# Optimization experiments

Hardware: AMD Instinct MI355X
Metric: run time of the kernel (lower is better)

The kernel has to match this reference:

```python
import jax, jax.numpy as jnp
import numpy as np

N_OUT, D_OUT, N_IN, D_IN, N_ROUTING = 32, 32, 2048, 16, 3
BATCH = 64


def squash(x, axis=-1):
    norm2 = jnp.sum(x * x, axis=axis, keepdims=True)
    scale = norm2 / (1.0 + norm2) / jnp.sqrt(norm2)
    return scale * x


def setup_inputs() -> dict:
    key = jax.random.key(0)
    k_u, k_w = jax.random.split(key)
    u = jax.random.normal(k_u, (BATCH, N_IN, D_IN), dtype=jnp.float32)
    stdv = 1.0 / np.sqrt(N_IN)
    W = jax.random.uniform(k_w, (N_IN, D_IN, N_OUT * D_OUT), dtype=jnp.float32,
                           minval=-stdv, maxval=stdv)
    return {"u": u, "W": W}


def reference(u, W):
    B = u.shape[0]
    # uhat[b,n,o,k] = sum_i u[b,n,i] * W[n,i,o*k]
    uhat = jnp.einsum('bni,nij->bnj', u, W).reshape(B, N_IN, N_OUT, D_OUT)
    b = jnp.zeros((B, N_IN, N_OUT), dtype=u.dtype)
    v = None
    for r in range(N_ROUTING):
        c = jax.nn.softmax(b, axis=-1)            # [B, nIn, nOut]
        s = jnp.einsum('bno,bnok->bok', c, uhat)  # [B, nOut, dOut]
        v = squash(s)
        if r != N_ROUTING - 1:
            a = jnp.einsum('bnok,bok->bno', uhat, v)  # agreement
            b = b + a
    return v
```

## Files before the change

kernel.cpp:

```cpp
#include <hip/hip_runtime.h>
#include <math.h>

#define N_OUT 32
#define D_OUT 32
#define N_IN 2048
#define D_IN 16
#define BATCH 64
#define J 1024

typedef __attribute__((ext_vector_type(8))) short short8;
typedef __attribute__((ext_vector_type(4))) float f32x4;
typedef __attribute__((ext_vector_type(16))) float f32x16;

__device__ __forceinline__ unsigned short f2bf(float f) {
  unsigned int x = __float_as_uint(f);
  return (unsigned short)((x + 0x7FFFu + ((x >> 16) & 1u)) >> 16);
}

__device__ __forceinline__ int wp(int u) { return u ^ ((u >> 3) & 1); }

__device__ __forceinline__ void pack_col(const float* wc, uint4& d0, uint4& d1) {
  d0.x = (unsigned)f2bf(wc[0])  | ((unsigned)f2bf(wc[1])  << 16);
  d0.y = (unsigned)f2bf(wc[2])  | ((unsigned)f2bf(wc[3])  << 16);
  d0.z = (unsigned)f2bf(wc[4])  | ((unsigned)f2bf(wc[5])  << 16);
  d0.w = (unsigned)f2bf(wc[6])  | ((unsigned)f2bf(wc[7])  << 16);
  d1.x = (unsigned)f2bf(wc[8])  | ((unsigned)f2bf(wc[9])  << 16);
  d1.y = (unsigned)f2bf(wc[10]) | ((unsigned)f2bf(wc[11]) << 16);
  d1.z = (unsigned)f2bf(wc[12]) | ((unsigned)f2bf(wc[13]) << 16);
  d1.w = (unsigned)f2bf(wc[14]) | ((unsigned)f2bf(wc[15]) << 16);
}

__device__ __forceinline__ short8 pack_u(const float4& a4, const float4& b4) {
  short8 B;
  B[0] = (short)f2bf(a4.x); B[1] = (short)f2bf(a4.y);
  B[2] = (short)f2bf(a4.z); B[3] = (short)f2bf(a4.w);
  B[4] = (short)f2bf(b4.x); B[5] = (short)f2bf(b4.y);
  B[6] = (short)f2bf(b4.z); B[7] = (short)f2bf(b4.w);
  return B;
}

__device__ __forceinline__ f32x16 zero16() {
  f32x16 z;
  #pragma unroll
  for (int i = 0; i < 16; ++i) z[i] = 0.f;
  return z;
}


template<int MODE>
__global__ __launch_bounds__(1024, 1)
void pass0w_kernel(const float* __restrict__ uf, const float* __restrict__ Wf,
                   short* __restrict__ Wbf, short* __restrict__ ubf,
                   float* __restrict__ part)
{
  __shared__ uint4 Wt[4][2048];

  const int t  = threadIdx.x;
  const int l  = t & 63;
  const int w  = t >> 6;
  const int bid = blockIdx.x;
  const int bh = (bid >> 3) & 1;
  const int cx = (bid & 7) | ((bid >> 4) << 3);
  const int n0 = cx * 16;

  const int bl = l & 31;
  const int b  = bh * 32 + bl;
  const int kh = l >> 5;
  const bool wq = (MODE == 0) && ((t >> 9) == bh);
  const bool uq = (MODE == 0) && (w == 0);

  int aoff[2];
  #pragma unroll
  for (int q = 0; q < 2; ++q) aoff[q] = wp(2 * (w * 64 + q * 32 + bl) + kh);

  f32x16 acc[2];
  acc[0] = zero16();
  acc[1] = zero16();

  short8 Ba, Bb;

  {
    float wa[16], wb[16];
    const float* sa = Wf + (size_t)n0 * (D_IN * J) + t;
    const float* sb = Wf + (size_t)(n0 + 1) * (D_IN * J) + t;
    #pragma unroll
    for (int i = 0; i < 16; ++i) wa[i] = sa[i * J];
    #pragma unroll
    for (int i = 0; i < 16; ++i) wb[i] = sb[i * J];
    const float* upa = uf + ((size_t)b * N_IN + n0) * D_IN + kh * 8;
    float4 ua0 = *reinterpret_cast<const float4*>(upa);
    float4 ua1 = *reinterpret_cast<const float4*>(upa + 4);
    const float* upb = uf + ((size_t)b * N_IN + n0 + 1) * D_IN + kh * 8;
    float4 ub0 = *reinterpret_cast<const float4*>(upb);
    float4 ub1 = *reinterpret_cast<const float4*>(upb + 4);
    __builtin_amdgcn_sched_barrier(0);
    uint4 d0, d1;
    pack_col(wa, d0, d1);
    Wt[0][wp(2 * t)] = d0;
    Wt[0][wp(2 * t + 1)] = d1;
    if (wq) {
      uint4* g = reinterpret_cast<uint4*>(Wbf + (size_t)n0 * (D_IN * J));
      g[wp(2 * t)] = d0;
      g[wp(2 * t + 1)] = d1;
    }
    pack_col(wb, d0, d1);
    Wt[1][wp(2 * t)] = d0;
    Wt[1][wp(2 * t + 1)] = d1;
    if (wq) {
      uint4* g = reinterpret_cast<uint4*>(Wbf + (size_t)(n0 + 1) * (D_IN * J));
      g[wp(2 * t)] = d0;
      g[wp(2 * t + 1)] = d1;
    }
    Ba = pack_u(ua0, ua1);
    Bb = pack_u(ub0, ub1);
    if (uq) {
      *reinterpret_cast<short8*>(ubf + ((size_t)b * N_IN + n0) * D_IN + kh * 8) = Ba;
      *reinterpret_cast<short8*>(ubf + ((size_t)b * N_IN + n0 + 1) * D_IN + kh * 8) = Bb;
    }
  }
  __syncthreads();

  for (int ss = 0; ss < 8; ++ss) {
    const int na = n0 + 2 * ss;
    const int p = ss & 1;
    const bool more = (ss + 1 < 8);

    float wa[16], wb[16];
    float4 ua0 = {0,0,0,0}, ua1 = {0,0,0,0}, ub0 = {0,0,0,0}, ub1 = {0,0,0,0};
    if (more) {
      const float* sa = Wf + (size_t)(na + 2) * (D_IN * J) + t;
      const float* sb = Wf + (size_t)(na + 3) * (D_IN * J) + t;
      #pragma unroll
      for (int i = 0; i < 16; ++i) wa[i] = sa[i * J];
      #pragma unroll
      for (int i = 0; i < 16; ++i) wb[i] = sb[i * J];
      const float* upa = uf + ((size_t)b * N_IN + na + 2) * D_IN + kh * 8;
      ua0 = *reinterpret_cast<const float4*>(upa);
      ua1 = *reinterpret_cast<const float4*>(upa + 4);
      const float* upb = uf + ((size_t)b * N_IN + na + 3) * D_IN + kh * 8;
      ub0 = *reinterpret_cast<const float4*>(upb);
      ub1 = *reinterpret_cast<const float4*>(upb + 4);
      __builtin_amdgcn_sched_barrier(0);
    }

    {
      const uint4* bufA = Wt[2 * p];
      const uint4* bufB = Wt[2 * p + 1];
      #pragma unroll
      for (int q = 0; q < 2; ++q) {
        short8 A = *reinterpret_cast<const short8*>(&bufA[aoff[q]]);
        acc[q] = __builtin_amdgcn_mfma_f32_32x32x16_bf16(A, Ba, acc[q], 0, 0, 0);
      }
      #pragma unroll
      for (int q = 0; q < 2; ++q) {
        short8 A = *reinterpret_cast<const short8*>(&bufB[aoff[q]]);
        acc[q] = __builtin_amdgcn_mfma_f32_32x32x16_bf16(A, Bb, acc[q], 0, 0, 0);
      }
    }

    short8 Bna, Bnb;
    if (more) {
      uint4 d0, d1;
      pack_col(wa, d0, d1);
      Wt[2 * (1 - p)][wp(2 * t)] = d0;
      Wt[2 * (1 - p)][wp(2 * t + 1)] = d1;
      if (wq) {
        uint4* g = reinterpret_cast<uint4*>(Wbf + (size_t)(na + 2) * (D_IN * J));
        g[wp(2 * t)] = d0;
        g[wp(2 * t + 1)] = d1;
      }
      pack_col(wb, d0, d1);
      Wt[2 * (1 - p) + 1][wp(2 * t)] = d0;
      Wt[2 * (1 - p) + 1][wp(2 * t + 1)] = d1;
      if (wq) {
        uint4* g = reinterpret_cast<uint4*>(Wbf + (size_t)(na + 3) * (D_IN * J));
        g[wp(2 * t)] = d0;
        g[wp(2 * t + 1)] = d1;
      }
      Bna = pack_u(ua0, ua1);
      Bnb = pack_u(ub0, ub1);
      if (uq) {
        *reinterpret_cast<short8*>(ubf + ((size_t)b * N_IN + na + 2) * D_IN + kh * 8) = Bna;
        *reinterpret_cast<short8*>(ubf + ((size_t)b * N_IN + na + 3) * D_IN + kh * 8) = Bnb;
      }
      Ba = Bna;
      Bb = Bnb;
    }
    __syncthreads();
  }

  #pragma unroll
  for (int q = 0; q < 2; ++q) {
    #pragma unroll
    for (int r = 0; r < 16; ++r) {
      int j = w * 64 + q * 32 + (r & 3) + 8 * (r >> 2) + 4 * kh;
      part[((size_t)cx * J + j) * 64 + b] = acc[q][r];
    }
  }
}

__global__ __launch_bounds__(1024, 1)
void pass1w_kernel(const short* __restrict__ Wbf, const short* __restrict__ ubf,
                   const float* __restrict__ vin, float* __restrict__ part)
{
  __shared__ uint4 Wt[2][2048];
  __shared__ float al[2][32][33];

  const int t  = threadIdx.x;
  const int l  = t & 63;
  const int w  = t >> 6;
  const int bid = blockIdx.x;
  const int bh = (bid >> 3) & 1;
  const int cx = (bid & 7) | ((bid >> 4) << 3);
  const int n0 = cx * 16;

  const int bl = l & 31;
  const int b  = bh * 32 + bl;
  const int kh = l >> 5;

  int aoff[2];
  #pragma unroll
  for (int q = 0; q < 2; ++q) aoff[q] = wp(2 * (w * 64 + q * 32 + bl) + kh);

  unsigned vb[16];
  #pragma unroll
  for (int q = 0; q < 2; ++q) {
    #pragma unroll
    for (int g = 0; g < 4; ++g) {
      int j = w * 64 + q * 32 + 8 * g + 4 * kh;
      f32x4 v4 = *reinterpret_cast<const f32x4*>(vin + (size_t)b * J + j);
      vb[q * 8 + 2 * g]     = (unsigned)f2bf(v4[0]) | ((unsigned)f2bf(v4[1]) << 16);
      vb[q * 8 + 2 * g + 1] = (unsigned)f2bf(v4[2]) | ((unsigned)f2bf(v4[3]) << 16);
    }
  }

  f32x16 acc[2];
  acc[0] = zero16();
  acc[1] = zero16();

  short8 B;
  {
    const uint4* src = reinterpret_cast<const uint4*>(Wbf + (size_t)n0 * (D_IN * J));
    Wt[0][t] = src[t];
    Wt[0][t + 1024] = src[t + 1024];
    B = *reinterpret_cast<const short8*>(ubf + ((size_t)b * N_IN + n0) * D_IN + kh * 8);
  }
  __syncthreads();

  for (int nn = 0; nn < 16; ++nn) {
    const int n = n0 + nn;
    const int cur = nn & 1, nxt = cur ^ 1, par = nn & 1;
    const bool more = (nn + 1 < 16);

    uint4 s0, s1;
    short8 Bn;
    if (more) {
      const uint4* src = reinterpret_cast<const uint4*>(Wbf + (size_t)(n + 1) * (D_IN * J));
      s0 = src[t];
      s1 = src[t + 1024];
      Bn = *reinterpret_cast<const short8*>(ubf + ((size_t)b * N_IN + n + 1) * D_IN + kh * 8);
      __builtin_amdgcn_sched_barrier(0);
    }

    f32x16 C[2];
    {
      const uint4* buf = Wt[cur];
      #pragma unroll
      for (int q = 0; q < 2; ++q) {
        short8 A = *reinterpret_cast<const short8*>(&buf[aoff[q]]);
        C[q] = __builtin_amdgcn_mfma_f32_32x32x16_bf16(A, B, zero16(), 0, 0, 0);
      }
    }

    #pragma unroll
    for (int q = 0; q < 2; ++q) {
      float s = 0.f;
      #pragma unroll
      for (int r = 0; r < 16; ++r) {
        unsigned u = vb[q * 8 + (r >> 1)];
        float v = (r & 1) ? __uint_as_float(u & 0xffff0000u)
                          : __uint_as_float(u << 16);
        s += C[q][r] * v;
      }
      s += __shfl_xor(s, 32);
      if (l < 32) al[par][w * 2 + q][bl] = s;
    }

    if (more) {
      Wt[nxt][t] = s0;
      Wt[nxt][t + 1024] = s1;
    }

    __syncthreads();
    {
      int sb = t >> 5, so = t & 31;
      float x = al[par][so][sb];
      float m = x;
      #pragma unroll
      for (int k = 1; k < 32; k <<= 1) m = fmaxf(m, __shfl_xor(m, k));
      float e = __expf(x - m);
      float sm = e;
      #pragma unroll
      for (int k = 1; k < 32; k <<= 1) sm += __shfl_xor(sm, k);
      al[par][so][sb] = e / sm;
    }
    __syncthreads();
    #pragma unroll
    for (int q = 0; q < 2; ++q) {
      float c = al[par][w * 2 + q][bl];
      #pragma unroll
      for (int r = 0; r < 16; ++r) acc[q][r] += C[q][r] * c;
    }
    B = Bn;
  }

  #pragma unroll
  for (int q = 0; q < 2; ++q) {
    #pragma unroll
    for (int r = 0; r < 16; ++r) {
      int j = w * 64 + q * 32 + (r & 3) + 8 * (r >> 2) + 4 * kh;
      part[((size_t)cx * J + j) * 64 + b] = acc[q][r];
    }
  }
}

template<int NC>
__global__ __launch_bounds__(1024)
void rsq_kernel(const float* __restrict__ part, const float* __restrict__ addv,
                float* __restrict__ out, float prescale)
{
  __shared__ float ps[2][32][17];
  __shared__ float vl[32][17];
  __shared__ float scl[16];
  const int o  = blockIdx.x >> 2;
  const int bq = blockIdx.x & 3;
  const int t  = threadIdx.x;
  {
    const int bb = t & 15;
    const int kk = (t >> 4) & 31;
    const int ch = t >> 9;
    const float* p = part + (size_t)(o * 32 + kk) * 64 + bq * 16 + bb;
    float s = 0.f;
    #pragma unroll 8
    for (int c = ch * (NC / 2); c < (ch + 1) * (NC / 2); ++c)
      s += p[(size_t)c * (J * 64)];
    ps[ch][kk][bb] = s;
  }
  __syncthreads();
  if (t < 512) {
    int kk = t >> 4, bb = t & 15;
    vl[kk][bb] = (ps[0][kk][bb] + ps[1][kk][bb]) * prescale;
  }
  __syncthreads();
  if (t < 16) {
    float n2 = 0.f;
    #pragma unroll
    for (int k = 0; k < 32; ++k) { float x = vl[k][t]; n2 += x * x; }
    scl[t] = sqrtf(n2) / (1.f + n2);
  }
  __syncthreads();
  if (t < 512) {
    int bb = t >> 5, kk = t & 31;
    int idx = (bq * 16 + bb) * J + o * 32 + kk;
    float val = scl[bb] * vl[kk][bb];
    if (addv) val += addv[idx];
    out[idx] = val;
  }
}

extern "C" void kernel_launch(void* const* d_in, const int* in_sizes, int n_in,
                              void* d_out, int out_size, void* d_ws, size_t ws_size,
                              hipStream_t stream)
{
  const float* u = (const float*)d_in[0];
  const float* W = (const float*)d_in[1];
  float* out = (float*)d_out;
  char* ws = (char*)d_ws;

  const size_t WBF_B = (size_t)N_IN * D_IN * J * 2;
  const size_t UBF_B = (size_t)BATCH * N_IN * D_IN * 2;
  const size_t SMALL = 2ull * BATCH * J * 4;
  const size_t PART128 = (size_t)128 * J * 64 * 4;

  short* Wbf = (short*)ws;
  short* ubf = (short*)(ws + WBF_B);
  float* part = (float*)(ws + WBF_B + UBF_B);
  float* v0 = part + (size_t)128 * J * 64;
  float* vs = v0 + BATCH * J;
  (void)PART128; (void)SMALL; (void)ws_size;

  pass0w_kernel<0><<<256, 1024, 0, stream>>>(u, W, Wbf, ubf, part);
  rsq_kernel<128><<<128, 1024, 0, stream>>>(part, nullptr, v0, 1.f / 32.f);
  pass1w_kernel<<<256, 1024, 0, stream>>>(Wbf, ubf, v0, part);
  rsq_kernel<128><<<128, 1024, 0, stream>>>(part, v0, vs, 1.f);
  pass1w_kernel<<<256, 1024, 0, stream>>>(Wbf, ubf, vs, part);
  rsq_kernel<128><<<128, 1024, 0, stream>>>(part, nullptr, out, 1.f);
}
```

Baseline: 165.7 us.

## Split first-pass kernel into 512-thread blocks over output-column halves

```diff
diff --git a/kernel.cpp b/kernel.cpp
--- a/kernel.cpp
+++ b/kernel.cpp
@@ -9,8 +9,8 @@
 #define J 1024
 
 typedef __attribute__((ext_vector_type(8))) short short8;
+typedef __attribute__((ext_vector_type(16))) float f32x16;
 typedef __attribute__((ext_vector_type(4))) float f32x4;
-typedef __attribute__((ext_vector_type(16))) float f32x16;
 
 __device__ __forceinline__ unsigned short f2bf(float f) {
   unsigned int x = __float_as_uint(f);
@@ -46,28 +46,28 @@
   return z;
 }
 
-
-template<int MODE>
-__global__ __launch_bounds__(1024, 1)
-void pass0w_kernel(const float* __restrict__ uf, const float* __restrict__ Wf,
-                   short* __restrict__ Wbf, short* __restrict__ ubf,
-                   float* __restrict__ part)
+__global__ __launch_bounds__(512, 4)
+void pass0w512_kernel(const float* __restrict__ uf, const float* __restrict__ Wf,
+                      short* __restrict__ Wbf, short* __restrict__ ubf,
+                      float* __restrict__ part)
 {
-  __shared__ uint4 Wt[4][2048];
+  __shared__ uint4 Wt[4][1024];
 
   const int t  = threadIdx.x;
   const int l  = t & 63;
   const int w  = t >> 6;
   const int bid = blockIdx.x;
-  const int bh = (bid >> 3) & 1;
-  const int cx = (bid & 7) | ((bid >> 4) << 3);
+  const int jh = (bid >> 3) & 1;
+  const int bh = (bid >> 4) & 1;
+  const int cx = (bid & 7) | ((bid >> 5) << 3);
   const int n0 = cx * 16;
 
   const int bl = l & 31;
   const int b  = bh * 32 + bl;
   const int kh = l >> 5;
-  const bool wq = (MODE == 0) && ((t >> 9) == bh);
-  const bool uq = (MODE == 0) && (w == 0);
+  const int jcol = jh * 512 + t;
+  const bool wq = (bh == 0);
+  const bool uq = (jh == 0) && (w == 0);
 
   int aoff[2];
   #pragma unroll
@@ -81,8 +81,8 @@
 
   {
     float wa[16], wb[16];
-    const float* sa = Wf + (size_t)n0 * (D_IN * J) + t;
-    const float* sb = Wf + (size_t)(n0 + 1) * (D_IN * J) + t;
+    const float* sa = Wf + (size_t)n0 * (D_IN * J) + jcol;
+    const float* sb = Wf + (size_t)(n0 + 1) * (D_IN * J) + jcol;
     #pragma unroll
     for (int i = 0; i < 16; ++i) wa[i] = sa[i * J];
     #pragma unroll
@@ -99,7 +99,7 @@
     Wt[0][wp(2 * t)] = d0;
     Wt[0][wp(2 * t + 1)] = d1;
     if (wq) {
-      uint4* g = reinterpret_cast<uint4*>(Wbf + (size_t)n0 * (D_IN * J));
+      uint4* g = reinterpret_cast<uint4*>(Wbf + (size_t)n0 * (D_IN * J)) + jh * 1024;
       g[wp(2 * t)] = d0;
       g[wp(2 * t + 1)] = d1;
     }
@@ -107,7 +107,7 @@
     Wt[1][wp(2 * t)] = d0;
     Wt[1][wp(2 * t + 1)] = d1;
     if (wq) {
-      uint4* g = reinterpret_cast<uint4*>(Wbf + (size_t)(n0 + 1) * (D_IN * J));
+      uint4* g = reinterpret_cast<uint4*>(Wbf + (size_t)(n0 + 1) * (D_IN * J)) + jh * 1024;
       g[wp(2 * t)] = d0;
       g[wp(2 * t + 1)] = d1;
     }
@@ -128,8 +128,8 @@
     float wa[16], wb[16];
     float4 ua0 = {0,0,0,0}, ua1 = {0,0,0,0}, ub0 = {0,0,0,0}, ub1 = {0,0,0,0};
     if (more) {
-      const float* sa = Wf + (size_t)(na + 2) * (D_IN * J) + t;
-      const float* sb = Wf + (size_t)(na + 3) * (D_IN * J) + t;
+      const float* sa = Wf + (size_t)(na + 2) * (D_IN * J) + jcol;
+      const float* sb = Wf + (size_t)(na + 3) * (D_IN * J) + jcol;
       #pragma unroll
       for (int i = 0; i < 16; ++i) wa[i] = sa[i * J];
       #pragma unroll
@@ -165,7 +165,7 @@
       Wt[2 * (1 - p)][wp(2 * t)] = d0;
       Wt[2 * (1 - p)][wp(2 * t + 1)] = d1;
       if (wq) {
-        uint4* g = reinterpret_cast<uint4*>(Wbf + (size_t)(na + 2) * (D_IN * J));
+        uint4* g = reinterpret_cast<uint4*>(Wbf + (size_t)(na + 2) * (D_IN * J)) + jh * 1024;
         g[wp(2 * t)] = d0;
         g[wp(2 * t + 1)] = d1;
       }
@@ -173,7 +173,7 @@
       Wt[2 * (1 - p) + 1][wp(2 * t)] = d0;
       Wt[2 * (1 - p) + 1][wp(2 * t + 1)] = d1;
       if (wq) {
-        uint4* g = reinterpret_cast<uint4*>(Wbf + (size_t)(na + 3) * (D_IN * J));
+        uint4* g = reinterpret_cast<uint4*>(Wbf + (size_t)(na + 3) * (D_IN * J)) + jh * 1024;
         g[wp(2 * t)] = d0;
         g[wp(2 * t + 1)] = d1;
       }
@@ -193,7 +193,7 @@
   for (int q = 0; q < 2; ++q) {
     #pragma unroll
     for (int r = 0; r < 16; ++r) {
-      int j = w * 64 + q * 32 + (r & 3) + 8 * (r >> 2) + 4 * kh;
+      int j = jh * 512 + w * 64 + q * 32 + (r & 3) + 8 * (r >> 2) + 4 * kh;
       part[((size_t)cx * J + j) * 64 + b] = acc[q][r];
     }
   }
@@ -379,17 +379,15 @@
 
   const size_t WBF_B = (size_t)N_IN * D_IN * J * 2;
   const size_t UBF_B = (size_t)BATCH * N_IN * D_IN * 2;
-  const size_t SMALL = 2ull * BATCH * J * 4;
-  const size_t PART128 = (size_t)128 * J * 64 * 4;
 
   short* Wbf = (short*)ws;
   short* ubf = (short*)(ws + WBF_B);
   float* part = (float*)(ws + WBF_B + UBF_B);
   float* v0 = part + (size_t)128 * J * 64;
   float* vs = v0 + BATCH * J;
-  (void)PART128; (void)SMALL; (void)ws_size;
-
-  pass0w_kernel<0><<<256, 1024, 0, stream>>>(u, W, Wbf, ubf, part);
+  (void)ws_size;
+
+  pass0w512_kernel<<<512, 512, 0, stream>>>(u, W, Wbf, ubf, part);
   rsq_kernel<128><<<128, 1024, 0, stream>>>(part, nullptr, v0, 1.f / 32.f);
   pass1w_kernel<<<256, 1024, 0, stream>>>(Wbf, ubf, v0, part);
   rsq_kernel<128><<<128, 1024, 0, stream>>>(part, v0, vs, 1.f);
```

Result: slower. 169.1 us (+2.0%).
